# Kernel optimization log

Measured on AMD Instinct MI355X. Metric: run time of the kernel, lower is better.

The kernel has to match this reference:

```python
import jax, jax.numpy as jnp
import numpy as np

B, H, W, C, NH, WS = 64, 56, 56, 128, 4, 7
N = H * W


def setup_inputs() -> dict:
    key = jax.random.key(0)
    ks = jax.random.split(key, 6)
    return {
        "x": jax.random.normal(ks[0], (B, N, C), jnp.float32),
        "w_qkv": jax.random.normal(ks[1], (3 * C, C), jnp.float32) * 0.02,
        "w_lim": jax.random.normal(ks[2], (C, 1, 3, 3), jnp.float32) * 0.02,
        "b_lim": jax.random.normal(ks[3], (C,), jnp.float32) * 0.02,
        "w_proj": jax.random.normal(ks[4], (C, C), jnp.float32) * 0.02,
        "b_proj": jax.random.normal(ks[5], (C,), jnp.float32) * 0.02,
        "H": H,
        "W": W,
    }


def reference(x, w_qkv, w_lim, b_lim, w_proj, b_proj, H, W):
    Bq, Nq, Cq = x.shape
    ws, nh = WS, NH
    hd = Cq // nh
    hg, wg = H // ws, W // ws  # 8, 8 -- no padding needed at these shapes
    scale = hd ** -0.5

    qkv = x @ w_qkv.T                      # (B, N, 3C)
    q, k, v = jnp.split(qkv, 3, axis=-1)

    def img2win(t):
        # (B,N,C) -> (B, hg*wg, nh, ws*ws, hd)
        t = t.reshape(Bq, hg, ws, wg, ws, Cq).transpose(0, 1, 3, 2, 4, 5)
        return t.reshape(Bq, hg * wg, ws * ws, nh, hd).transpose(0, 1, 3, 2, 4)

    qw, kw, vw = img2win(q), img2win(k), img2win(v)

    # LIM: depthwise 3x3 conv on shape-integrated V (win2img(img2win(v)) == v as NCHW)
    v_img = v.reshape(Bq, H, W, Cq).transpose(0, 3, 1, 2)     # (B,C,H,W)
    v_lim = jax.lax.conv_general_dilated(
        v_img, w_lim, window_strides=(1, 1), padding='SAME',
        dimension_numbers=('NCHW', 'OIHW', 'NCHW'), feature_group_count=Cq)
    v_lim = v_lim + b_lim[None, :, None, None]
    v_lim = v_lim.reshape(Bq, Cq, Nq).transpose(0, 2, 1)      # (B,N,C)

    # windowed attention: g = window index, n = head
    attn = jax.nn.softmax(
        jnp.einsum('bgnqd,bgnkd->bgnqk', qw, kw) * scale, axis=-1)
    out = jnp.einsum('bgnqk,bgnkd->bgnqd', attn, vw)          # (B,g,nh,ws*ws,hd)

    # merge windows back: (B,g,nh,ws*ws,hd) -> (B,N,C)
    out = out.transpose(0, 1, 3, 2, 4).reshape(Bq, hg, wg, ws, ws, Cq)
    out = out.transpose(0, 1, 3, 2, 4, 5).reshape(Bq, Nq, Cq)

    out = out + v_lim
    return out @ w_proj.T + b_proj
```

## Files before the change

### kernel.cpp

```cpp
#include <hip/hip_runtime.h>
#include <cstdint>

#define B_   64
#define H_   56
#define W_   56
#define C_   128
#define WSZ  7
#define TT   49
#define NN   3136
#define MM   (B_ * NN)
#define SCALE 0.17677669529663687f

typedef short bf16x8 __attribute__((ext_vector_type(8)));
typedef short bf16x4 __attribute__((ext_vector_type(4)));
typedef float f32x4  __attribute__((ext_vector_type(4)));
typedef unsigned short u16;

__device__ __forceinline__ float bf2f(u16 u) {
    return __uint_as_float(((unsigned int)u) << 16);
}
__device__ __forceinline__ u16 f2bf(float f) {
    unsigned int u = __float_as_uint(f);
    u += 0x7FFFu + ((u >> 16) & 1u);
    return (u16)(u >> 16);
}

__global__ __launch_bounds__(256) void kw_cvt(
    const float* __restrict__ wqkv, const float* __restrict__ wproj,
    u16* __restrict__ wqbf, u16* __restrict__ wpbf)
{
    int g = blockIdx.x * 256 + threadIdx.x;
    if (g < 12288) {
        float4 f = *(const float4*)&wqkv[g * 4];
        float mul = (g < 4096) ? SCALE : 1.0f;
        ushort4 u;
        u.x = f2bf(f.x * mul); u.y = f2bf(f.y * mul);
        u.z = f2bf(f.z * mul); u.w = f2bf(f.w * mul);
        *(ushort4*)&wqbf[g * 4] = u;
    } else {
        int g2 = g - 12288;
        float4 f = *(const float4*)&wproj[g2 * 4];
        ushort4 u;
        u.x = f2bf(f.x); u.y = f2bf(f.y);
        u.z = f2bf(f.z); u.w = f2bf(f.w);
        *(ushort4*)&wpbf[g2 * 4] = u;
    }
}

template <bool PREW>
__global__ __launch_bounds__(256, 3) void ka_fused(
    const float* __restrict__ x, const float* __restrict__ wqkv,
    const u16* __restrict__ wqbf,
    u16* __restrict__ vout, float* __restrict__ out)
{
    __shared__ u16 lds[26240];
    u16 (*xq)[136] = (u16(*)[136])&lds[0];
    u16 (*ks)[136] = (u16(*)[136])&lds[8704];
    u16 (*vs)[138] = (u16(*)[138])&lds[17408];
    u16* ps_ = &lds[0];

    const int t   = threadIdx.x;
    const int blk = blockIdx.x;
    const int b_  = blk >> 6, wr = blk & 63;
    const int qy  = wr >> 3, qx = wr & 7;
    const int wave = t >> 6, lane = t & 63, lr = lane & 15, quad = lane >> 4;

    for (int i = t; i < 64 * 32; i += 256) {
        int tok = i >> 5, c4 = (i & 31) * 4;
        ushort4 u4 = {0, 0, 0, 0};
        if (tok < TT) {
            int hh = qy * WSZ + tok / WSZ, ww = qx * WSZ + tok % WSZ;
            float4 f = *(const float4*)&x[((size_t)b_ * NN + hh * W_ + ww) * C_ + c4];
            u4.x = f2bf(f.x); u4.y = f2bf(f.y);
            u4.z = f2bf(f.z); u4.w = f2bf(f.w);
        }
        *(ushort4*)&xq[tok][c4] = u4;
    }
    __syncthreads();

#pragma unroll
    for (int cc = 0; cc < 2; cc++) {
        const int ch = 1 + cc;
        u16* dstbase = cc ? &vs[0][0] : &ks[0][0];
        const int dstride = cc ? 138 : 136;
#pragma unroll
        for (int half = 0; half < 2; half++) {
            const int wrowi = ch * 128 + half * 64 + wave * 16 + lr;
            const float* wrowf = &wqkv[(size_t)wrowi * C_];
            const u16*   wrowb = &wqbf[(size_t)wrowi * C_];
            f32x4 acc[4];
#pragma unroll
            for (int mi = 0; mi < 4; mi++) acc[mi] = {0.f, 0.f, 0.f, 0.f};
#pragma unroll
            for (int kk = 0; kk < 4; kk++) {
                bf16x8 bfr;
                if constexpr (PREW) {
                    bfr = *(const bf16x8*)&wrowb[kk * 32 + quad * 8];
                } else {
                    float4 f0 = *(const float4*)&wrowf[kk * 32 + quad * 8];
                    float4 f1 = *(const float4*)&wrowf[kk * 32 + quad * 8 + 4];
                    bfr[0] = (short)f2bf(f0.x); bfr[1] = (short)f2bf(f0.y);
                    bfr[2] = (short)f2bf(f0.z); bfr[3] = (short)f2bf(f0.w);
                    bfr[4] = (short)f2bf(f1.x); bfr[5] = (short)f2bf(f1.y);
                    bfr[6] = (short)f2bf(f1.z); bfr[7] = (short)f2bf(f1.w);
                }
#pragma unroll
                for (int mi = 0; mi < 4; mi++) {
                    bf16x8 afr = *(const bf16x8*)&xq[mi * 16 + lr][kk * 32 + quad * 8];
                    acc[mi] = __builtin_amdgcn_mfma_f32_16x16x32_bf16(
                        afr, bfr, acc[mi], 0, 0, 0);
                }
            }
#pragma unroll
            for (int mi = 0; mi < 4; mi++) {
#pragma unroll
                for (int r = 0; r < 4; r++) {
                    int tok = mi * 16 + quad * 4 + r;
                    int col = half * 64 + wave * 16 + lr;
                    u16 bv = f2bf(acc[mi][r]);
                    dstbase[tok * dstride + col] = bv;
                    if (cc == 1 && tok < TT) {
                        int hh2 = qy * WSZ + tok / WSZ;
                        int ww2 = qx * WSZ + tok % WSZ;
                        vout[((size_t)b_ * NN + hh2 * W_ + ww2) * C_ + col] = bv;
                    }
                }
            }
        }
    }

    const float qmul = PREW ? 1.0f : SCALE;
    f32x4 qacc[2][4];
#pragma unroll
    for (int half = 0; half < 2; half++)
#pragma unroll
        for (int mi = 0; mi < 4; mi++) qacc[half][mi] = {0.f, 0.f, 0.f, 0.f};
#pragma unroll
    for (int half = 0; half < 2; half++) {
        const int wrowi = half * 64 + wave * 16 + lr;
        const float* wrowf = &wqkv[(size_t)wrowi * C_];
        const u16*   wrowb = &wqbf[(size_t)wrowi * C_];
#pragma unroll
        for (int kk = 0; kk < 4; kk++) {
            bf16x8 bfr;
            if constexpr (PREW) {
                bfr = *(const bf16x8*)&wrowb[kk * 32 + quad * 8];
            } else {
                float4 f0 = *(const float4*)&wrowf[kk * 32 + quad * 8];
                float4 f1 = *(const float4*)&wrowf[kk * 32 + quad * 8 + 4];
                bfr[0] = (short)f2bf(f0.x); bfr[1] = (short)f2bf(f0.y);
                bfr[2] = (short)f2bf(f0.z); bfr[3] = (short)f2bf(f0.w);
                bfr[4] = (short)f2bf(f1.x); bfr[5] = (short)f2bf(f1.y);
                bfr[6] = (short)f2bf(f1.z); bfr[7] = (short)f2bf(f1.w);
            }
#pragma unroll
            for (int mi = 0; mi < 4; mi++) {
                bf16x8 afr = *(const bf16x8*)&xq[mi * 16 + lr][kk * 32 + quad * 8];
                qacc[half][mi] = __builtin_amdgcn_mfma_f32_16x16x32_bf16(
                    afr, bfr, qacc[half][mi], 0, 0, 0);
            }
        }
    }
    __syncthreads();

#pragma unroll
    for (int half = 0; half < 2; half++)
#pragma unroll
        for (int mi = 0; mi < 4; mi++)
#pragma unroll
            for (int r = 0; r < 4; r++)
                xq[mi * 16 + quad * 4 + r][half * 64 + wave * 16 + lr] =
                    f2bf(qacc[half][mi][r] * qmul);
    __syncthreads();

    const int h = wave;
    bf16x8 qf[4], kf[4];
#pragma unroll
    for (int mi = 0; mi < 4; mi++) {
        qf[mi] = *(const bf16x8*)&xq[mi * 16 + lr][h * 32 + quad * 8];
        kf[mi] = *(const bf16x8*)&ks[mi * 16 + lr][h * 32 + quad * 8];
    }
    __syncthreads();

    f32x4 s[4][4];
#pragma unroll
    for (int mi = 0; mi < 4; mi++)
#pragma unroll
        for (int nj = 0; nj < 4; nj++) s[mi][nj] = {0.f, 0.f, 0.f, 0.f};
#pragma unroll
    for (int mi = 0; mi < 4; mi++)
#pragma unroll
        for (int nj = 0; nj < 4; nj++)
            s[mi][nj] = __builtin_amdgcn_mfma_f32_16x16x32_bf16(
                qf[mi], kf[nj], s[mi][nj], 0, 0, 0);

    if (lr >= 1) {
#pragma unroll
        for (int mi = 0; mi < 4; mi++)
#pragma unroll
            for (int r = 0; r < 4; r++) s[mi][3][r] = -1e30f;
    }

    float rsum[4][4];
#pragma unroll
    for (int mi = 0; mi < 4; mi++) {
#pragma unroll
        for (int r = 0; r < 4; r++) {
            float mx = fmaxf(fmaxf(s[mi][0][r], s[mi][1][r]),
                             fmaxf(s[mi][2][r], s[mi][3][r]));
#pragma unroll
            for (int off = 1; off < 16; off <<= 1)
                mx = fmaxf(mx, __shfl_xor(mx, off));
            float sum = 0.f;
#pragma unroll
            for (int nj = 0; nj < 4; nj++) {
                float p = __expf(s[mi][nj][r] - mx);
                s[mi][nj][r] = p;
                sum += p;
            }
#pragma unroll
            for (int off = 1; off < 16; off <<= 1)
                sum += __shfl_xor(sum, off);
            rsum[mi][r] = sum;
        }
    }

#pragma unroll
    for (int mi = 0; mi < 4; mi++)
#pragma unroll
        for (int nj = 0; nj < 4; nj++)
#pragma unroll
            for (int r = 0; r < 4; r++)
                ps_[((h * 64) + mi * 16 + quad * 4 + r) * 68 + nj * 16 + lr] =
                    f2bf(s[mi][nj][r]);

    f32x4 o[4][2];
#pragma unroll
    for (int mi = 0; mi < 4; mi++)
#pragma unroll
        for (int nv = 0; nv < 2; nv++) o[mi][nv] = {0.f, 0.f, 0.f, 0.f};

#pragma unroll
    for (int kt = 0; kt < 2; kt++) {
        bf16x8 pf[4];
#pragma unroll
        for (int mi = 0; mi < 4; mi++) {
            const u16* pp = &ps_[((h * 64) + mi * 16 + lr) * 68 + kt * 32 + quad * 8];
            bf16x4 lo = *(const bf16x4*)&pp[0];
            bf16x4 hi = *(const bf16x4*)&pp[4];
            bf16x8 f;
            f[0] = lo[0]; f[1] = lo[1]; f[2] = lo[2]; f[3] = lo[3];
            f[4] = hi[0]; f[5] = hi[1]; f[6] = hi[2]; f[7] = hi[3];
            pf[mi] = f;
        }
        bf16x8 vf[2];
#pragma unroll
        for (int nv = 0; nv < 2; nv++) {
            bf16x8 tmp;
#pragma unroll
            for (int jj = 0; jj < 8; jj++)
                tmp[jj] = (short)vs[kt * 32 + quad * 8 + jj][h * 32 + nv * 16 + lr];
            vf[nv] = tmp;
        }
#pragma unroll
        for (int mi = 0; mi < 4; mi++)
#pragma unroll
            for (int nv = 0; nv < 2; nv++)
                o[mi][nv] = __builtin_amdgcn_mfma_f32_16x16x32_bf16(
                    pf[mi], vf[nv], o[mi][nv], 0, 0, 0);
    }

#pragma unroll
    for (int mi = 0; mi < 4; mi++) {
#pragma unroll
        for (int r = 0; r < 4; r++) {
            int i = mi * 16 + quad * 4 + r;
            if (i < TT) {
                int hh = qy * WSZ + i / WSZ, ww = qx * WSZ + i % WSZ;
                size_t orow = (size_t)b_ * NN + hh * W_ + ww;
                float inv = 1.f / rsum[mi][r];
#pragma unroll
                for (int nv = 0; nv < 2; nv++)
                    out[orow * C_ + h * 32 + nv * 16 + lr] = o[mi][nv][r] * inv;
            }
        }
    }
}

template <bool ZOUT>
__global__ __launch_bounds__(256) void kb_lim(
    const u16* __restrict__ v, const float* __restrict__ wlim,
    const float* __restrict__ blim, const float* __restrict__ y,
    u16* __restrict__ z, float* __restrict__ out)
{
    const int t   = threadIdx.x;
    const int pos = blockIdx.x * 16 + (t >> 4);
    const int c0  = (t & 15) * 8;
    const int b_  = pos / NN;
    const int rem = pos - b_ * NN;
    const int hh  = rem / W_;
    const int ww  = rem - hh * W_;

    float w72[72];
    {
        const float* wp = &wlim[c0 * 9];
#pragma unroll
        for (int i = 0; i < 18; i++) {
            float4 f = *(const float4*)&wp[i * 4];
            w72[i * 4 + 0] = f.x; w72[i * 4 + 1] = f.y;
            w72[i * 4 + 2] = f.z; w72[i * 4 + 3] = f.w;
        }
    }
    float acc[8];
    {
        float4 b0 = *(const float4*)&blim[c0];
        float4 b1 = *(const float4*)&blim[c0 + 4];
        acc[0] = b0.x; acc[1] = b0.y; acc[2] = b0.z; acc[3] = b0.w;
        acc[4] = b1.x; acc[5] = b1.y; acc[6] = b1.z; acc[7] = b1.w;
    }

    const u16* vbase = &v[(size_t)b_ * NN * C_ + c0];
#pragma unroll
    for (int dy = -1; dy <= 1; dy++) {
        int yy = hh + dy;
        bool yok = (unsigned)yy < (unsigned)H_;
#pragma unroll
        for (int dx = -1; dx <= 1; dx++) {
            int x2 = ww + dx;
            bool ok = yok && ((unsigned)x2 < (unsigned)W_);
            bf16x8 vv = {0, 0, 0, 0, 0, 0, 0, 0};
            if (ok) vv = *(const bf16x8*)&vbase[(size_t)(yy * W_ + x2) * C_];
            const int tap = (dy + 1) * 3 + (dx + 1);
#pragma unroll
            for (int j = 0; j < 8; j++)
                acc[j] += bf2f((u16)vv[j]) * w72[j * 9 + tap];
        }
    }

    if constexpr (ZOUT) {
        const float* yp = &y[(size_t)pos * C_ + c0];
        float4 y0 = *(const float4*)&yp[0];
        float4 y1 = *(const float4*)&yp[4];
        bf16x8 zz;
        zz[0] = (short)f2bf(y0.x + acc[0]); zz[1] = (short)f2bf(y0.y + acc[1]);
        zz[2] = (short)f2bf(y0.z + acc[2]); zz[3] = (short)f2bf(y0.w + acc[3]);
        zz[4] = (short)f2bf(y1.x + acc[4]); zz[5] = (short)f2bf(y1.y + acc[5]);
        zz[6] = (short)f2bf(y1.z + acc[6]); zz[7] = (short)f2bf(y1.w + acc[7]);
        *(bf16x8*)&z[(size_t)pos * C_ + c0] = zz;
    } else {
        float* op = &out[(size_t)pos * C_ + c0];
        float4 o0 = *(const float4*)&op[0];
        float4 o1 = *(const float4*)&op[4];
        o0.x += acc[0]; o0.y += acc[1]; o0.z += acc[2]; o0.w += acc[3];
        o1.x += acc[4]; o1.y += acc[5]; o1.z += acc[6]; o1.w += acc[7];
        *(float4*)&op[0] = o0;
        *(float4*)&op[4] = o1;
    }
}

template <int MODE>
__global__ __launch_bounds__(256) void kc_proj(
    float* __restrict__ y, const u16* __restrict__ z,
    const float* __restrict__ wproj, const u16* __restrict__ wpbf,
    const float* __restrict__ bproj)
{
    __shared__ u16 As[128][72];
    __shared__ u16 Ws[128][72];
    const int t    = threadIdx.x;
    const int m0   = blockIdx.x * 128;
    const int wave = t >> 6, lane = t & 63, lr = lane & 15, quad = lane >> 4;
    const int wm = (wave >> 1) * 64, wn = (wave & 1) * 64;

    f32x4 acc[4][4];
#pragma unroll
    for (int mi = 0; mi < 4; mi++)
#pragma unroll
        for (int ni = 0; ni < 4; ni++) acc[mi][ni] = {0.f, 0.f, 0.f, 0.f};

#pragma unroll
    for (int kt = 0; kt < 2; kt++) {
        const int k0 = kt * 64;

        if constexpr (MODE == 2) {
#pragma unroll
            for (int p4 = 0; p4 < 4; p4++) {
                int e    = p4 * 256 + t;
                int row  = e >> 3;
                int col8 = (e & 7) * 8;
                *(bf16x8*)&As[row][col8] =
                    *(const bf16x8*)&z[(size_t)(m0 + row) * C_ + k0 + col8];
            }
        } else {
#pragma unroll
            for (int p = 0; p < 8; p++) {
                int e   = p * 256 + t;
                int row = e >> 4;
                int col = (e & 15) * 4;
                float4 fa = *(const float4*)&y[(size_t)(m0 + row) * C_ + k0 + col];
                ushort4 ua;
                ua.x = f2bf(fa.x); ua.y = f2bf(fa.y);
                ua.z = f2bf(fa.z); ua.w = f2bf(fa.w);
                *(ushort4*)&As[row][col] = ua;
            }
        }

        if constexpr (MODE >= 1) {
#pragma unroll
            for (int p4 = 0; p4 < 4; p4++) {
                int e    = p4 * 256 + t;
                int row  = e >> 3;
                int col8 = (e & 7) * 8;
                *(bf16x8*)&Ws[row][col8] =
                    *(const bf16x8*)&wpbf[(size_t)row * C_ + k0 + col8];
            }
        } else {
#pragma unroll
            for (int p = 0; p < 8; p++) {
                int e   = p * 256 + t;
                int row = e >> 4;
                int col = (e & 15) * 4;
                float4 fw = *(const float4*)&wproj[(size_t)row * C_ + k0 + col];
                ushort4 uw;
                uw.x = f2bf(fw.x); uw.y = f2bf(fw.y);
                uw.z = f2bf(fw.z); uw.w = f2bf(fw.w);
                *(ushort4*)&Ws[row][col] = uw;
            }
        }
        __syncthreads();
#pragma unroll
        for (int kk = 0; kk < 2; kk++) {
            bf16x8 a[4], b[4];
#pragma unroll
            for (int mi = 0; mi < 4; mi++)
                a[mi] = *(const bf16x8*)&As[wm + mi * 16 + lr][kk * 32 + quad * 8];
#pragma unroll
            for (int ni = 0; ni < 4; ni++)
                b[ni] = *(const bf16x8*)&Ws[wn + ni * 16 + lr][kk * 32 + quad * 8];
#pragma unroll
            for (int mi = 0; mi < 4; mi++)
#pragma unroll
                for (int ni = 0; ni < 4; ni++)
                    acc[mi][ni] = __builtin_amdgcn_mfma_f32_16x16x32_bf16(
                        a[mi], b[ni], acc[mi][ni], 0, 0, 0);
        }
        if (kt == 0) __syncthreads();
    }

#pragma unroll
    for (int mi = 0; mi < 4; mi++) {
#pragma unroll
        for (int r = 0; r < 4; r++) {
            int m = m0 + wm + mi * 16 + quad * 4 + r;
#pragma unroll
            for (int ni = 0; ni < 4; ni++) {
                int c = wn + ni * 16 + lr;
                y[(size_t)m * C_ + c] = acc[mi][ni][r] + bproj[c];
            }
        }
    }
}

extern "C" void kernel_launch(void* const* d_in, const int* in_sizes, int n_in,
                              void* d_out, int out_size, void* d_ws, size_t ws_size,
                              hipStream_t stream)
{
    const float* x     = (const float*)d_in[0];
    const float* wqkv  = (const float*)d_in[1];
    const float* wlim  = (const float*)d_in[2];
    const float* blim  = (const float*)d_in[3];
    const float* wproj = (const float*)d_in[4];
    const float* bproj = (const float*)d_in[5];
    float* out = (float*)d_out;
    u16*   v   = (u16*)d_ws;

    const size_t vbytes = (size_t)MM * C_ * 2;
    const size_t wbytes = (49152 + 16384) * 2;
    const size_t need1  = vbytes + wbytes;
    const size_t need2  = need1 + vbytes;

    if (ws_size >= need2) {
        u16* wqbf = (u16*)((char*)d_ws + vbytes);
        u16* wpbf = wqbf + 49152;
        u16* zbuf = (u16*)((char*)d_ws + need1);
        kw_cvt<<<dim3(64), 256, 0, stream>>>(wqkv, wproj, wqbf, wpbf);
        ka_fused<true><<<dim3(B_ * 64), 256, 0, stream>>>(x, wqkv, wqbf, v, out);
        kb_lim<true><<<dim3(MM / 16), 256, 0, stream>>>(v, wlim, blim, out, zbuf, nullptr);
        kc_proj<2><<<dim3(MM / 128), 256, 0, stream>>>(out, zbuf, nullptr, wpbf, bproj);
    } else if (ws_size >= need1) {
        u16* wqbf = (u16*)((char*)d_ws + vbytes);
        u16* wpbf = wqbf + 49152;
        kw_cvt<<<dim3(64), 256, 0, stream>>>(wqkv, wproj, wqbf, wpbf);
        ka_fused<true><<<dim3(B_ * 64), 256, 0, stream>>>(x, wqkv, wqbf, v, out);
        kb_lim<false><<<dim3(MM / 16), 256, 0, stream>>>(v, wlim, blim, nullptr, nullptr, out);
        kc_proj<1><<<dim3(MM / 128), 256, 0, stream>>>(out, nullptr, nullptr, wpbf, bproj);
    } else {
        ka_fused<false><<<dim3(B_ * 64), 256, 0, stream>>>(x, wqkv, nullptr, v, out);
        kb_lim<false><<<dim3(MM / 16), 256, 0, stream>>>(v, wlim, blim, nullptr, nullptr, out);
        kc_proj<0><<<dim3(MM / 128), 256, 0, stream>>>(out, nullptr, wproj, nullptr, bproj);
    }
}
```

Measured before the change: 380.4 us.

## Store attention output as bf16, add LIM in place, use LDS-free projection

Result: no change. 386.8 us (+1.7%).

```diff
diff --git a/kernel.cpp b/kernel.cpp
--- a/kernel.cpp
+++ b/kernel.cpp
@@ -47,11 +47,11 @@
     }
 }
 
-template <bool PREW>
+template <bool PREW, bool YBF>
 __global__ __launch_bounds__(256, 3) void ka_fused(
     const float* __restrict__ x, const float* __restrict__ wqkv,
     const u16* __restrict__ wqbf,
-    u16* __restrict__ vout, float* __restrict__ out)
+    u16* __restrict__ vout, u16* __restrict__ ybf, float* __restrict__ out)
 {
     __shared__ u16 lds[26240];
     u16 (*xq)[136] = (u16(*)[136])&lds[0];
@@ -280,18 +280,23 @@
                 size_t orow = (size_t)b_ * NN + hh * W_ + ww;
                 float inv = 1.f / rsum[mi][r];
 #pragma unroll
-                for (int nv = 0; nv < 2; nv++)
-                    out[orow * C_ + h * 32 + nv * 16 + lr] = o[mi][nv][r] * inv;
-            }
-        }
-    }
-}
-
-template <bool ZOUT>
+                for (int nv = 0; nv < 2; nv++) {
+                    float val = o[mi][nv][r] * inv;
+                    if constexpr (YBF)
+                        ybf[orow * C_ + h * 32 + nv * 16 + lr] = f2bf(val);
+                    else
+                        out[orow * C_ + h * 32 + nv * 16 + lr] = val;
+                }
+            }
+        }
+    }
+}
+
+template <bool INPLACE>
 __global__ __launch_bounds__(256) void kb_lim(
     const u16* __restrict__ v, const float* __restrict__ wlim,
-    const float* __restrict__ blim, const float* __restrict__ y,
-    u16* __restrict__ z, float* __restrict__ out)
+    const float* __restrict__ blim, u16* __restrict__ z,
+    float* __restrict__ out)
 {
     const int t   = threadIdx.x;
     const int pos = blockIdx.x * 16 + (t >> 4);
@@ -301,6 +306,15 @@
     const int hh  = rem / W_;
     const int ww  = rem - hh * W_;
 
+    bf16x8 yv;
+    float4 o0, o1;
+    if constexpr (INPLACE) {
+        yv = *(const bf16x8*)&z[(size_t)pos * C_ + c0];
+    } else {
+        o0 = *(const float4*)&out[(size_t)pos * C_ + c0];
+        o1 = *(const float4*)&out[(size_t)pos * C_ + c0 + 4];
+    }
+
     float w72[72];
     {
         const float* wp = &wlim[c0 * 9];
@@ -337,32 +351,74 @@
         }
     }
 
-    if constexpr (ZOUT) {
-        const float* yp = &y[(size_t)pos * C_ + c0];
-        float4 y0 = *(const float4*)&yp[0];
-        float4 y1 = *(const float4*)&yp[4];
+    if constexpr (INPLACE) {
         bf16x8 zz;
-        zz[0] = (short)f2bf(y0.x + acc[0]); zz[1] = (short)f2bf(y0.y + acc[1]);
-        zz[2] = (short)f2bf(y0.z + acc[2]); zz[3] = (short)f2bf(y0.w + acc[3]);
-        zz[4] = (short)f2bf(y1.x + acc[4]); zz[5] = (short)f2bf(y1.y + acc[5]);
-        zz[6] = (short)f2bf(y1.z + acc[6]); zz[7] = (short)f2bf(y1.w + acc[7]);
+#pragma unroll
+        for (int j = 0; j < 8; j++)
+            zz[j] = (short)f2bf(bf2f((u16)yv[j]) + acc[j]);
         *(bf16x8*)&z[(size_t)pos * C_ + c0] = zz;
     } else {
-        float* op = &out[(size_t)pos * C_ + c0];
-        float4 o0 = *(const float4*)&op[0];
-        float4 o1 = *(const float4*)&op[4];
         o0.x += acc[0]; o0.y += acc[1]; o0.z += acc[2]; o0.w += acc[3];
         o1.x += acc[4]; o1.y += acc[5]; o1.z += acc[6]; o1.w += acc[7];
-        *(float4*)&op[0] = o0;
-        *(float4*)&op[4] = o1;
+        *(float4*)&out[(size_t)pos * C_ + c0]     = o0;
+        *(float4*)&out[(size_t)pos * C_ + c0 + 4] = o1;
+    }
+}
+
+__global__ __launch_bounds__(256, 4) void kc_direct(
+    const u16* __restrict__ z, const u16* __restrict__ wpbf,
+    const float* __restrict__ bproj, float* __restrict__ out)
+{
+    const int t    = threadIdx.x;
+    const int m0   = blockIdx.x * 128;
+    const int wave = t >> 6, lane = t & 63, lr = lane & 15, quad = lane >> 4;
+    const int wm = (wave >> 1) * 64, wn = (wave & 1) * 64;
+
+    f32x4 acc[4][4];
+#pragma unroll
+    for (int mi = 0; mi < 4; mi++)
+#pragma unroll
+        for (int ni = 0; ni < 4; ni++) acc[mi][ni] = {0.f, 0.f, 0.f, 0.f};
+
+#pragma unroll
+    for (int kt = 0; kt < 2; kt++) {
+#pragma unroll
+        for (int kk = 0; kk < 2; kk++) {
+            const int kcol = kt * 64 + kk * 32 + quad * 8;
+            bf16x8 a[4], b[4];
+#pragma unroll
+            for (int mi = 0; mi < 4; mi++)
+                a[mi] = *(const bf16x8*)&z[(size_t)(m0 + wm + mi * 16 + lr) * C_ + kcol];
+#pragma unroll
+            for (int ni = 0; ni < 4; ni++)
+                b[ni] = *(const bf16x8*)&wpbf[(size_t)(wn + ni * 16 + lr) * C_ + kcol];
+#pragma unroll
+            for (int mi = 0; mi < 4; mi++)
+#pragma unroll
+                for (int ni = 0; ni < 4; ni++)
+                    acc[mi][ni] = __builtin_amdgcn_mfma_f32_16x16x32_bf16(
+                        a[mi], b[ni], acc[mi][ni], 0, 0, 0);
+        }
+    }
+
+#pragma unroll
+    for (int mi = 0; mi < 4; mi++) {
+#pragma unroll
+        for (int r = 0; r < 4; r++) {
+            int m = m0 + wm + mi * 16 + quad * 4 + r;
+#pragma unroll
+            for (int ni = 0; ni < 4; ni++) {
+                int c = wn + ni * 16 + lr;
+                out[(size_t)m * C_ + c] = acc[mi][ni][r] + bproj[c];
+            }
+        }
     }
 }
 
 template <int MODE>
 __global__ __launch_bounds__(256) void kc_proj(
-    float* __restrict__ y, const u16* __restrict__ z,
-    const float* __restrict__ wproj, const u16* __restrict__ wpbf,
-    const float* __restrict__ bproj)
+    float* __restrict__ y, const float* __restrict__ wproj,
+    const u16* __restrict__ wpbf, const float* __restrict__ bproj)
 {
     __shared__ u16 As[128][72];
     __shared__ u16 Ws[128][72];
@@ -380,30 +436,24 @@
 #pragma unroll
     for (int kt = 0; kt < 2; kt++) {
         const int k0 = kt * 64;
-
-        if constexpr (MODE == 2) {
-#pragma unroll
-            for (int p4 = 0; p4 < 4; p4++) {
-                int e    = p4 * 256 + t;
-                int row  = e >> 3;
-                int col8 = (e & 7) * 8;
-                *(bf16x8*)&As[row][col8] =
-                    *(const bf16x8*)&z[(size_t)(m0 + row) * C_ + k0 + col8];
-            }
-        } else {
-#pragma unroll
-            for (int p = 0; p < 8; p++) {
-                int e   = p * 256 + t;
-                int row = e >> 4;
-                int col = (e & 15) * 4;
-                float4 fa = *(const float4*)&y[(size_t)(m0 + row) * C_ + k0 + col];
-                ushort4 ua;
-                ua.x = f2bf(fa.x); ua.y = f2bf(fa.y);
-                ua.z = f2bf(fa.z); ua.w = f2bf(fa.w);
-                *(ushort4*)&As[row][col] = ua;
-            }
-        }
-
+#pragma unroll
+        for (int p = 0; p < 8; p++) {
+            int e   = p * 256 + t;
+            int row = e >> 4;
+            int col = (e & 15) * 4;
+            float4 fa = *(const float4*)&y[(size_t)(m0 + row) * C_ + k0 + col];
+            ushort4 ua;
+            ua.x = f2bf(fa.x); ua.y = f2bf(fa.y);
+            ua.z = f2bf(fa.z); ua.w = f2bf(fa.w);
+            *(ushort4*)&As[row][col] = ua;
+            if constexpr (MODE == 0) {
+                float4 fw = *(const float4*)&wproj[(size_t)row * C_ + k0 + col];
+                ushort4 uw;
+                uw.x = f2bf(fw.x); uw.y = f2bf(fw.y);
+                uw.z = f2bf(fw.z); uw.w = f2bf(fw.w);
+                *(ushort4*)&Ws[row][col] = uw;
+            }
+        }
         if constexpr (MODE >= 1) {
 #pragma unroll
             for (int p4 = 0; p4 < 4; p4++) {
@@ -412,18 +462,6 @@
                 int col8 = (e & 7) * 8;
                 *(bf16x8*)&Ws[row][col8] =
                     *(const bf16x8*)&wpbf[(size_t)row * C_ + k0 + col8];
-            }
-        } else {
-#pragma unroll
-            for (int p = 0; p < 8; p++) {
-                int e   = p * 256 + t;
-                int row = e >> 4;
-                int col = (e & 15) * 4;
-                float4 fw = *(const float4*)&wproj[(size_t)row * C_ + k0 + col];
-                ushort4 uw;
-                uw.x = f2bf(fw.x); uw.y = f2bf(fw.y);
-                uw.z = f2bf(fw.z); uw.w = f2bf(fw.w);
-                *(ushort4*)&Ws[row][col] = uw;
             }
         }
         __syncthreads();
@@ -483,19 +521,22 @@
         u16* wpbf = wqbf + 49152;
         u16* zbuf = (u16*)((char*)d_ws + need1);
         kw_cvt<<<dim3(64), 256, 0, stream>>>(wqkv, wproj, wqbf, wpbf);
-        ka_fused<true><<<dim3(B_ * 64), 256, 0, stream>>>(x, wqkv, wqbf, v, out);
-        kb_lim<true><<<dim3(MM / 16), 256, 0, stream>>>(v, wlim, blim, out, zbuf, nullptr);
-        kc_proj<2><<<dim3(MM / 128), 256, 0, stream>>>(out, zbuf, nullptr, wpbf, bproj);
+        ka_fused<true, true><<<dim3(B_ * 64), 256, 0, stream>>>(
+            x, wqkv, wqbf, v, zbuf, nullptr);
+        kb_lim<true><<<dim3(MM / 16), 256, 0, stream>>>(v, wlim, blim, zbuf, nullptr);
+        kc_direct<<<dim3(MM / 128), 256, 0, stream>>>(zbuf, wpbf, bproj, out);
     } else if (ws_size >= need1) {
         u16* wqbf = (u16*)((char*)d_ws + vbytes);
         u16* wpbf = wqbf + 49152;
         kw_cvt<<<dim3(64), 256, 0, stream>>>(wqkv, wproj, wqbf, wpbf);
-        ka_fused<true><<<dim3(B_ * 64), 256, 0, stream>>>(x, wqkv, wqbf, v, out);
-        kb_lim<false><<<dim3(MM / 16), 256, 0, stream>>>(v, wlim, blim, nullptr, nullptr, out);
-        kc_proj<1><<<dim3(MM / 128), 256, 0, stream>>>(out, nullptr, nullptr, wpbf, bproj);
+        ka_fused<true, false><<<dim3(B_ * 64), 256, 0, stream>>>(
+            x, wqkv, wqbf, v, nullptr, out);
+        kb_lim<false><<<dim3(MM / 16), 256, 0, stream>>>(v, wlim, blim, nullptr, out);
+        kc_proj<1><<<dim3(MM / 128), 256, 0, stream>>>(out, nullptr, wpbf, bproj);
     } else {
-        ka_fused<false><<<dim3(B_ * 64), 256, 0, stream>>>(x, wqkv, nullptr, v, out);
-        kb_lim<false><<<dim3(MM / 16), 256, 0, stream>>>(v, wlim, blim, nullptr, nullptr, out);
-        kc_proj<0><<<dim3(MM / 128), 256, 0, stream>>>(out, nullptr, wproj, nullptr, bproj);
-    }
-}
+        ka_fused<false, false><<<dim3(B_ * 64), 256, 0, stream>>>(
+            x, wqkv, nullptr, v, nullptr, out);
+        kb_lim<false><<<dim3(MM / 16), 256, 0, stream>>>(v, wlim, blim, nullptr, out);
+        kc_proj<0><<<dim3(MM / 128), 256, 0, stream>>>(out, wproj, nullptr, bproj);
+    }
+}
```
